# Performance work log

Hardware: AMD Instinct MI355X
Metric: run time of the kernel (lower is better)

Reference implementation:

```python
import jax, jax.numpy as jnp
import numpy as np

N_NODES = 100000

def spmm(edge_row, edge_col, edge_val, dense):
    # sparse [N,N] @ dense [N,D] via gather + segment_sum
    msgs = edge_val[:, None] * dense[edge_col]          # [E, D]
    return jax.ops.segment_sum(msgs, edge_row, num_segments=N_NODES)

def setup_inputs() -> dict:
    key = jax.random.key(0)
    ks = jax.random.split(key, 6)
    N, F, H, C, E = N_NODES, 512, 256, 40, 3200000
    x = jax.random.normal(ks[0], (N, F), dtype=jnp.float32)
    edge_row = jax.random.randint(ks[1], (E,), 0, N, dtype=jnp.int32)
    edge_col = jax.random.randint(ks[2], (E,), 0, N, dtype=jnp.int32)
    edge_val = jax.random.uniform(ks[3], (E,), dtype=jnp.float32)
    # xavier_uniform init for conv weights, zeros for biases
    lim1 = float(np.sqrt(6.0 / (F + H)))
    lim2 = float(np.sqrt(6.0 / (H + C)))
    W1 = jax.random.uniform(ks[4], (F, H), minval=-lim1, maxval=lim1, dtype=jnp.float32)
    b1 = jnp.zeros((H,), dtype=jnp.float32)
    W2 = jax.random.uniform(ks[5], (H, C), minval=-lim2, maxval=lim2, dtype=jnp.float32)
    b2 = jnp.zeros((C,), dtype=jnp.float32)
    return {"x": x, "edge_row": edge_row, "edge_col": edge_col, "edge_val": edge_val,
            "W1": W1, "b1": b1, "W2": W2, "b2": b2}

def reference(x, edge_row, edge_col, edge_val, W1, b1, W2, b2):
    # layer 1: dense transform, sparse aggregation, bias, relu (dropout = identity in eval)
    h = spmm(edge_row, edge_col, edge_val, x @ W1) + b1   # [N, H]
    h = jax.nn.relu(h)
    mid = h
    # layer 2
    out = spmm(edge_row, edge_col, edge_val, h @ W2) + b2  # [N, C]
    return (mid, out)  # out.squeeze(1) is a no-op for C>1
```

## Files before the change

### kernel.cpp

```cpp
#include <hip/hip_runtime.h>


typedef __bf16 bf16;
typedef __bf16 bf16x8 __attribute__((ext_vector_type(8)));
typedef float floatx4 __attribute__((ext_vector_type(4)));
typedef float floatx2 __attribute__((ext_vector_type(2)));

#define NBMAX 400

__device__ __forceinline__ float bflo(unsigned int u) { return __uint_as_float(u << 16); }
__device__ __forceinline__ float bfhi(unsigned int u) { return __uint_as_float(u & 0xffff0000u); }

__global__ __launch_bounds__(256) void conv_w(const float* __restrict__ W1,
                                              const float* __restrict__ W2,
                                              bf16* __restrict__ W1T,
                                              bf16* __restrict__ W2T) {
  int i = blockIdx.x * 256 + threadIdx.x;
  if (i < 512 * 256) {
    int k = i >> 8, n = i & 255;
    W1T[n * 512 + k] = (bf16)W1[i];
  }
  int j = i - 512 * 256;
  if (j >= 0 && j < 48 * 256) {
    int n = j >> 8, k = j & 255;
    W2T[j] = (n < 40) ? (bf16)W2[k * 40 + n] : (bf16)0.0f;
  }
}

__global__ __launch_bounds__(256) void cvt_fp8_kernel(const unsigned int* __restrict__ in,
                                                      unsigned int* __restrict__ out,
                                                      int n8) {
  int i = blockIdx.x * 256 + threadIdx.x;
  if (i >= n8) return;
  uint4 u = ((const uint4*)in)[i];
  int p0 = 0, p1 = 0;
  p0 = __builtin_amdgcn_cvt_pk_fp8_f32(bflo(u.x), bfhi(u.x), p0, false);
  p0 = __builtin_amdgcn_cvt_pk_fp8_f32(bflo(u.y), bfhi(u.y), p0, true);
  p1 = __builtin_amdgcn_cvt_pk_fp8_f32(bflo(u.z), bfhi(u.z), p1, false);
  p1 = __builtin_amdgcn_cvt_pk_fp8_f32(bflo(u.w), bfhi(u.w), p1, true);
  ((uint2*)out)[i] = make_uint2((unsigned int)p0, (unsigned int)p1);
}

__global__ __launch_bounds__(256) void bhist_kernel(const int* __restrict__ er,
                                                    int* __restrict__ gbcount,
                                                    int E, int NB) {
  __shared__ int cnt[NBMAX];
  const int t = threadIdx.x;
  for (int b = t; b < NB; b += 256) cnt[b] = 0;
  __syncthreads();
  const int base = blockIdx.x * 8192;
#pragma unroll
  for (int k = 0; k < 8; k++) {
    int i = base + k * 1024 + t * 4;
    if (i < E) {
      int4 r = *(const int4*)(er + i);
      atomicAdd(&cnt[r.x >> 8], 1);
      atomicAdd(&cnt[r.y >> 8], 1);
      atomicAdd(&cnt[r.z >> 8], 1);
      atomicAdd(&cnt[r.w >> 8], 1);
    }
  }
  __syncthreads();
  for (int b = t; b < NB; b += 256)
    if (cnt[b]) atomicAdd(&gbcount[b], cnt[b]);
}

__global__ __launch_bounds__(512) void bscan_kernel(const int* __restrict__ gbcount,
                                                    int* __restrict__ bstart,
                                                    int* __restrict__ bcur, int NB) {
  __shared__ int wsum[8];
  const int t = threadIdx.x;
  const int lane = t & 63, wave = t >> 6;
  int v = (t < NB) ? gbcount[t] : 0;
  int incl = v;
#pragma unroll
  for (int d = 1; d < 64; d <<= 1) {
    int o = __shfl_up(incl, d, 64);
    if (lane >= d) incl += o;
  }
  if (lane == 63) wsum[wave] = incl;
  __syncthreads();
  int off = 0;
#pragma unroll
  for (int w = 0; w < 8; w++)
    if (w < wave) off += wsum[w];
  int excl = off + incl - v;
  if (t <= NB) bstart[t] = excl;
  if (t < NB) bcur[t] = excl;
}

__global__ __launch_bounds__(256) void partA_kernel(
    const int* __restrict__ er, const int* __restrict__ ec, const float* __restrict__ ev,
    int* __restrict__ bcur, int2* __restrict__ epack_b, int E, int NB) {
  __shared__ int cnt[NBMAX];
  __shared__ int cur[NBMAX];
  const int t = threadIdx.x;
  for (int b = t; b < NB; b += 256) cnt[b] = 0;
  __syncthreads();
  const int base = blockIdx.x * 8192;
#pragma unroll
  for (int k = 0; k < 8; k++) {
    int i = base + k * 1024 + t * 4;
    if (i < E) {
      int4 r = *(const int4*)(er + i);
      atomicAdd(&cnt[r.x >> 8], 1);
      atomicAdd(&cnt[r.y >> 8], 1);
      atomicAdd(&cnt[r.z >> 8], 1);
      atomicAdd(&cnt[r.w >> 8], 1);
    }
  }
  __syncthreads();
  for (int b = t; b < NB; b += 256)
    cur[b] = cnt[b] ? atomicAdd(&bcur[b], cnt[b]) : 0;
  __syncthreads();
#pragma unroll
  for (int k = 0; k < 8; k++) {
    int i = base + k * 1024 + t * 4;
    if (i < E) {
      int4 r = *(const int4*)(er + i);
      int4 c = *(const int4*)(ec + i);
      float4 v = *(const float4*)(ev + i);
      int s0 = atomicAdd(&cur[r.x >> 8], 1);
      epack_b[s0] = make_int2(((r.x & 255) << 17) | c.x, __float_as_int(v.x));
      int s1 = atomicAdd(&cur[r.y >> 8], 1);
      epack_b[s1] = make_int2(((r.y & 255) << 17) | c.y, __float_as_int(v.y));
      int s2 = atomicAdd(&cur[r.z >> 8], 1);
      epack_b[s2] = make_int2(((r.z & 255) << 17) | c.z, __float_as_int(v.z));
      int s3 = atomicAdd(&cur[r.w >> 8], 1);
      epack_b[s3] = make_int2(((r.w & 255) << 17) | c.w, __float_as_int(v.w));
    }
  }
}

__global__ __launch_bounds__(256) void partB_kernel(
    const int2* __restrict__ epack_b, const int* __restrict__ bstart,
    int2* __restrict__ epack_f, int* __restrict__ rp, int M) {
  __shared__ int rcnt[256];
  __shared__ int rcur[256];
  __shared__ int wsum[4];
  const int b = blockIdx.x, t = threadIdx.x;
  const int s = bstart[b];
  const int e_ = bstart[b + 1];
  rcnt[t] = 0;
  __syncthreads();
  for (int i = s + t; i < e_; i += 256) {
    unsigned int ro = ((unsigned int)epack_b[i].x) >> 17;
    atomicAdd(&rcnt[ro], 1);
  }
  __syncthreads();
  const int lane = t & 63, wave = t >> 6;
  int v = rcnt[t];
  int incl = v;
#pragma unroll
  for (int d = 1; d < 64; d <<= 1) {
    int o = __shfl_up(incl, d, 64);
    if (lane >= d) incl += o;
  }
  if (lane == 63) wsum[wave] = incl;
  __syncthreads();
  int off = 0;
#pragma unroll
  for (int w = 0; w < 4; w++)
    if (w < wave) off += wsum[w];
  rcur[t] = s + off + incl - v;
  __syncthreads();
  for (int i = s + t; i < e_; i += 256) {
    int2 m = epack_b[i];
    unsigned int ro = ((unsigned int)m.x) >> 17;
    int slot = atomicAdd(&rcur[ro], 1);
    epack_f[slot] = make_int2(m.x & 0x1FFFF, m.y);
  }
  __syncthreads();
  int r = (b << 8) + t;
  if (r < M) rp[r] = rcur[t];
}

__global__ __launch_bounds__(256) void gemm1_kernel(const float* __restrict__ x,
                                                    const bf16* __restrict__ W1T,
                                                    bf16* __restrict__ T1, int M) {
  __shared__ __align__(16) bf16 As[64][40];
  __shared__ __align__(16) bf16 Bs[256][40];
  const int t = threadIdx.x;
  const int wave = t >> 6, lane = t & 63;
  const int quad = lane >> 4, l16 = lane & 15;
  const int m0 = blockIdx.x * 64;
  floatx4 acc[16] = {};

  const int ar = t >> 2, aq = t & 3;
  const int a_gr = m0 + ar;
  const float* a_src = x + (size_t)a_gr * 512 + aq * 8;
  const bf16* b_src = W1T + (size_t)t * 512;

  for (int k0 = 0; k0 < 512; k0 += 32) {
    __syncthreads();
    {
      float4 f0 = {0,0,0,0}, f1 = {0,0,0,0};
      if (a_gr < M) {
        const float4* p = (const float4*)(a_src + k0);
        f0 = p[0]; f1 = p[1];
      }
      bf16x8 av;
      av[0] = (bf16)f0.x; av[1] = (bf16)f0.y; av[2] = (bf16)f0.z; av[3] = (bf16)f0.w;
      av[4] = (bf16)f1.x; av[5] = (bf16)f1.y; av[6] = (bf16)f1.z; av[7] = (bf16)f1.w;
      *(bf16x8*)&As[ar][aq * 8] = av;
    }
    {
      const bf16* p = b_src + k0;
      bf16x8 q0 = *(const bf16x8*)(p);
      bf16x8 q1 = *(const bf16x8*)(p + 8);
      bf16x8 q2 = *(const bf16x8*)(p + 16);
      bf16x8 q3 = *(const bf16x8*)(p + 24);
      *(bf16x8*)&Bs[t][0]  = q0;
      *(bf16x8*)&Bs[t][8]  = q1;
      *(bf16x8*)&Bs[t][16] = q2;
      *(bf16x8*)&Bs[t][24] = q3;
    }
    __syncthreads();
    bf16x8 a = *(const bf16x8*)&As[wave * 16 + l16][quad * 8];
#pragma unroll
    for (int nt = 0; nt < 16; nt++) {
      bf16x8 b = *(const bf16x8*)&Bs[nt * 16 + l16][quad * 8];
      acc[nt] = __builtin_amdgcn_mfma_f32_16x16x32_bf16(a, b, acc[nt], 0, 0, 0);
    }
  }
  const int row_base = m0 + wave * 16 + quad * 4;
#pragma unroll
  for (int nt = 0; nt < 16; nt++) {
#pragma unroll
    for (int j = 0; j < 4; j++) {
      int gr = row_base + j;
      if (gr < M) T1[(size_t)gr * 256 + nt * 16 + l16] = (bf16)acc[nt][j];
    }
  }
}

__global__ __launch_bounds__(256) void spmm1_kernel(
    const int* __restrict__ rp, const int2* __restrict__ epack,
    const unsigned int* __restrict__ T1f8, const float* __restrict__ b1,
    float* __restrict__ mid, int M) {
  const int lane = threadIdx.x & 63;
  const int r = blockIdx.x * 4 + (threadIdx.x >> 6);
  if (r >= M) return;
  const int eend = rp[r];
  int e = (r == 0) ? 0 : rp[r - 1];
  float a0 = 0.f, a1 = 0.f, a2 = 0.f, a3 = 0.f;
  const unsigned int* base = T1f8 + lane;
  if (e < eend && (e & 1)) {
    int2 m = epack[e];
    float v = __int_as_float(m.y);
    unsigned int u = base[(size_t)m.x * 64];
    floatx2 lo = __builtin_amdgcn_cvt_pk_f32_fp8(u, false);
    floatx2 hi = __builtin_amdgcn_cvt_pk_f32_fp8(u, true);
    a0 += v * lo[0]; a1 += v * lo[1]; a2 += v * hi[0]; a3 += v * hi[1];
    e++;
  }
  for (; e + 3 < eend; e += 4) {
    int4 p01 = *(const int4*)(epack + e);
    int4 p23 = *(const int4*)(epack + e + 2);
    unsigned int u0 = base[(size_t)p01.x * 64];
    unsigned int u1 = base[(size_t)p01.z * 64];
    unsigned int u2 = base[(size_t)p23.x * 64];
    unsigned int u3 = base[(size_t)p23.z * 64];
    float v0 = __int_as_float(p01.y), v1 = __int_as_float(p01.w);
    float v2 = __int_as_float(p23.y), v3 = __int_as_float(p23.w);
    floatx2 l0 = __builtin_amdgcn_cvt_pk_f32_fp8(u0, false);
    floatx2 h0 = __builtin_amdgcn_cvt_pk_f32_fp8(u0, true);
    floatx2 l1 = __builtin_amdgcn_cvt_pk_f32_fp8(u1, false);
    floatx2 h1 = __builtin_amdgcn_cvt_pk_f32_fp8(u1, true);
    floatx2 l2 = __builtin_amdgcn_cvt_pk_f32_fp8(u2, false);
    floatx2 h2 = __builtin_amdgcn_cvt_pk_f32_fp8(u2, true);
    floatx2 l3 = __builtin_amdgcn_cvt_pk_f32_fp8(u3, false);
    floatx2 h3 = __builtin_amdgcn_cvt_pk_f32_fp8(u3, true);
    a0 += v0 * l0[0]; a1 += v0 * l0[1]; a2 += v0 * h0[0]; a3 += v0 * h0[1];
    a0 += v1 * l1[0]; a1 += v1 * l1[1]; a2 += v1 * h1[0]; a3 += v1 * h1[1];
    a0 += v2 * l2[0]; a1 += v2 * l2[1]; a2 += v2 * h2[0]; a3 += v2 * h2[1];
    a0 += v3 * l3[0]; a1 += v3 * l3[1]; a2 += v3 * h3[0]; a3 += v3 * h3[1];
  }
  for (; e < eend; e++) {
    int2 m = epack[e];
    float v = __int_as_float(m.y);
    unsigned int u = base[(size_t)m.x * 64];
    floatx2 lo = __builtin_amdgcn_cvt_pk_f32_fp8(u, false);
    floatx2 hi = __builtin_amdgcn_cvt_pk_f32_fp8(u, true);
    a0 += v * lo[0]; a1 += v * lo[1]; a2 += v * hi[0]; a3 += v * hi[1];
  }
  int c = lane * 4;
  float4 bb = *(const float4*)(b1 + c);
  float4 o;
  o.x = fmaxf(a0 + bb.x, 0.f);
  o.y = fmaxf(a1 + bb.y, 0.f);
  o.z = fmaxf(a2 + bb.z, 0.f);
  o.w = fmaxf(a3 + bb.w, 0.f);
  *(float4*)(mid + (size_t)r * 256 + c) = o;
}

__global__ __launch_bounds__(256) void gemm2_kernel(const float* __restrict__ mid,
                                                    const bf16* __restrict__ W2T,
                                                    bf16* __restrict__ T2p, int M) {
  __shared__ __align__(16) bf16 As[64][40];
  __shared__ __align__(16) bf16 Bs[48][40];
  const int t = threadIdx.x;
  const int wave = t >> 6, lane = t & 63;
  const int quad = lane >> 4, l16 = lane & 15;
  const int m0 = blockIdx.x * 64;
  floatx4 acc[3] = {};
  const int ar = t >> 2, aq = t & 3;
  const int a_gr = m0 + ar;
  const float* a_src = mid + (size_t)a_gr * 256 + aq * 8;

  for (int k0 = 0; k0 < 256; k0 += 32) {
    __syncthreads();
    {
      float4 f0 = {0,0,0,0}, f1 = {0,0,0,0};
      if (a_gr < M) {
        const float4* p = (const float4*)(a_src + k0);
        f0 = p[0]; f1 = p[1];
      }
      bf16x8 av;
      av[0] = (bf16)f0.x; av[1] = (bf16)f0.y; av[2] = (bf16)f0.z; av[3] = (bf16)f0.w;
      av[4] = (bf16)f1.x; av[5] = (bf16)f1.y; av[6] = (bf16)f1.z; av[7] = (bf16)f1.w;
      *(bf16x8*)&As[ar][aq * 8] = av;
    }
    if (t < 192) {
      int n = t >> 2, q = t & 3;
      bf16x8 b = *(const bf16x8*)(W2T + n * 256 + k0 + q * 8);
      *(bf16x8*)&Bs[n][q * 8] = b;
    }
    __syncthreads();
    bf16x8 a = *(const bf16x8*)&As[wave * 16 + l16][quad * 8];
#pragma unroll
    for (int nt = 0; nt < 3; nt++) {
      bf16x8 b = *(const bf16x8*)&Bs[nt * 16 + l16][quad * 8];
      acc[nt] = __builtin_amdgcn_mfma_f32_16x16x32_bf16(a, b, acc[nt], 0, 0, 0);
    }
  }
  const int row_base = m0 + wave * 16 + quad * 4;
#pragma unroll
  for (int nt = 0; nt < 3; nt++) {
#pragma unroll
    for (int j = 0; j < 4; j++) {
      int gr = row_base + j;
      int col = nt * 16 + l16;
      if (gr < M && col < 40) T2p[(size_t)gr * 64 + col] = (bf16)acc[nt][j];
    }
  }
}

__global__ __launch_bounds__(256) void spmm2_kernel(
    const int* __restrict__ rp, const int2* __restrict__ epack,
    const unsigned int* __restrict__ T2f8, const float* __restrict__ b2,
    float* __restrict__ out2, int M) {
  const int lane = threadIdx.x & 63;
  const int r = blockIdx.x * 4 + (threadIdx.x >> 6);
  if (r >= M) return;
  const int q = lane & 15;
  const int g = lane >> 4;
  const int eend = rp[r];
  int e = (r == 0) ? 0 : rp[r - 1];
  float a0 = 0.f, a1 = 0.f, a2 = 0.f, a3 = 0.f;
  const unsigned int* base = T2f8 + q;
  for (; e + 3 < eend; e += 4) {
    int2 m = epack[e + g];
    float v = __int_as_float(m.y);
    unsigned int u = base[(size_t)m.x * 16];
    floatx2 lo = __builtin_amdgcn_cvt_pk_f32_fp8(u, false);
    floatx2 hi = __builtin_amdgcn_cvt_pk_f32_fp8(u, true);
    a0 += v * lo[0]; a1 += v * lo[1]; a2 += v * hi[0]; a3 += v * hi[1];
  }
  if (e + g < eend) {
    int2 m = epack[e + g];
    float v = __int_as_float(m.y);
    unsigned int u = base[(size_t)m.x * 16];
    floatx2 lo = __builtin_amdgcn_cvt_pk_f32_fp8(u, false);
    floatx2 hi = __builtin_amdgcn_cvt_pk_f32_fp8(u, true);
    a0 += v * lo[0]; a1 += v * lo[1]; a2 += v * hi[0]; a3 += v * hi[1];
  }
  a0 += __shfl_down(a0, 32, 64); a0 += __shfl_down(a0, 16, 64);
  a1 += __shfl_down(a1, 32, 64); a1 += __shfl_down(a1, 16, 64);
  a2 += __shfl_down(a2, 32, 64); a2 += __shfl_down(a2, 16, 64);
  a3 += __shfl_down(a3, 32, 64); a3 += __shfl_down(a3, 16, 64);
  if (lane < 10) {
    int c = lane * 4;
    float4 o;
    o.x = a0 + b2[c];
    o.y = a1 + b2[c + 1];
    o.z = a2 + b2[c + 2];
    o.w = a3 + b2[c + 3];
    *(float4*)(out2 + (size_t)r * 40 + c) = o;
  }
}

extern "C" void kernel_launch(void* const* d_in, const int* in_sizes, int n_in,
                              void* d_out, int out_size, void* d_ws, size_t ws_size,
                              hipStream_t stream) {
  const float* x        = (const float*)d_in[0];
  const int*   edge_row = (const int*)d_in[1];
  const int*   edge_col = (const int*)d_in[2];
  const float* edge_val = (const float*)d_in[3];
  const float* W1       = (const float*)d_in[4];
  const float* b1       = (const float*)d_in[5];
  const float* W2       = (const float*)d_in[6];
  const float* b2       = (const float*)d_in[7];
  const int M = in_sizes[0] / 512;
  const int E = in_sizes[1];
  const int NB = (M + 255) >> 8;

  char* ws = (char*)d_ws;
  size_t off = 0;
  bf16* T1      = (bf16*)(ws + off);  off += (size_t)M * 256 * 2;
  bf16* W1T     = (bf16*)(ws + off);  off += 512 * 256 * 2;
  bf16* W2T     = (bf16*)(ws + off);  off += 48 * 256 * 2;
  bf16* T2p     = (bf16*)(ws + off);  off += (size_t)M * 64 * 2;
  unsigned int* T1f8 = (unsigned int*)(ws + off); off += (size_t)M * 256;
  unsigned int* T2f8 = (unsigned int*)(ws + off); off += (size_t)M * 64;
  int* rp       = (int*)(ws + off);   off += (size_t)M * 4;
  int* gbcount  = (int*)(ws + off);   off += NBMAX * 4;
  int* bstart   = (int*)(ws + off);   off += (NBMAX + 1) * 4;
  int* bcur     = (int*)(ws + off);   off += NBMAX * 4;
  off = (off + 15) & ~(size_t)15;
  int2* epack_f = (int2*)(ws + off);  off += (size_t)E * 8;
  int2* epack_b = (int2*)T1;

  float* mid  = (float*)d_out;
  float* out2 = mid + (size_t)M * 256;

  const int EBLK = (E + 8191) / 8192;

  hipMemsetAsync(gbcount, 0, NBMAX * 4, stream);
  conv_w<<<(512 * 256 + 48 * 256 + 255) / 256, 256, 0, stream>>>(W1, W2, W1T, W2T);
  bhist_kernel<<<EBLK, 256, 0, stream>>>(edge_row, gbcount, E, NB);
  bscan_kernel<<<1, 512, 0, stream>>>(gbcount, bstart, bcur, NB);
  partA_kernel<<<EBLK, 256, 0, stream>>>(edge_row, edge_col, edge_val,
                                         bcur, epack_b, E, NB);
  partB_kernel<<<NB, 256, 0, stream>>>(epack_b, bstart, epack_f, rp, M);
  gemm1_kernel<<<(M + 63) / 64, 256, 0, stream>>>(x, W1T, T1, M);
  {
    int n8 = M * 256 / 8;
    cvt_fp8_kernel<<<(n8 + 255) / 256, 256, 0, stream>>>((const unsigned int*)T1,
                                                         T1f8, n8);
  }
  spmm1_kernel<<<(M + 3) / 4, 256, 0, stream>>>(rp, epack_f, T1f8, b1, mid, M);
  gemm2_kernel<<<(M + 63) / 64, 256, 0, stream>>>(mid, W2T, T2p, M);
  {
    int n8 = M * 64 / 8;
    cvt_fp8_kernel<<<(n8 + 255) / 256, 256, 0, stream>>>((const unsigned int*)T2p,
                                                         T2f8, n8);
  }
  spmm2_kernel<<<(M + 3) / 4, 256, 0, stream>>>(rp, epack_f, T2f8, b2, out2, M);
}
```

Measured before the change: 737.6 us.

## Precompute per-block bucket offsets and unroll SpMM gather loops further

New measurement: 691.4 us. 6.3% less time.

```diff
diff --git a/kernel.cpp b/kernel.cpp
--- a/kernel.cpp
+++ b/kernel.cpp
@@ -43,7 +43,8 @@
 
 __global__ __launch_bounds__(256) void bhist_kernel(const int* __restrict__ er,
                                                     int* __restrict__ gbcount,
-                                                    int E, int NB) {
+                                                    int* __restrict__ blkcnt,
+                                                    int E, int NB, int EBLK) {
   __shared__ int cnt[NBMAX];
   const int t = threadIdx.x;
   for (int b = t; b < NB; b += 256) cnt[b] = 0;
@@ -61,13 +62,15 @@
     }
   }
   __syncthreads();
-  for (int b = t; b < NB; b += 256)
-    if (cnt[b]) atomicAdd(&gbcount[b], cnt[b]);
+  for (int b = t; b < NB; b += 256) {
+    int c = cnt[b];
+    blkcnt[b * EBLK + blockIdx.x] = c;
+    if (c) atomicAdd(&gbcount[b], c);
+  }
 }
 
 __global__ __launch_bounds__(512) void bscan_kernel(const int* __restrict__ gbcount,
-                                                    int* __restrict__ bstart,
-                                                    int* __restrict__ bcur, int NB) {
+                                                    int* __restrict__ bstart, int NB) {
   __shared__ int wsum[8];
   const int t = threadIdx.x;
   const int lane = t & 63, wave = t >> 6;
@@ -86,33 +89,38 @@
     if (w < wave) off += wsum[w];
   int excl = off + incl - v;
   if (t <= NB) bstart[t] = excl;
-  if (t < NB) bcur[t] = excl;
+}
+
+__global__ __launch_bounds__(512) void bscan2_kernel(const int* __restrict__ blkcnt,
+                                                     const int* __restrict__ bstart,
+                                                     int* __restrict__ blkoff, int EBLK) {
+  __shared__ int wsum[8];
+  const int b = blockIdx.x, t = threadIdx.x;
+  const int lane = t & 63, wave = t >> 6;
+  int v = (t < EBLK) ? blkcnt[b * EBLK + t] : 0;
+  int incl = v;
+#pragma unroll
+  for (int d = 1; d < 64; d <<= 1) {
+    int o = __shfl_up(incl, d, 64);
+    if (lane >= d) incl += o;
+  }
+  if (lane == 63) wsum[wave] = incl;
+  __syncthreads();
+  int off = 0;
+#pragma unroll
+  for (int w = 0; w < 8; w++)
+    if (w < wave) off += wsum[w];
+  if (t < EBLK) blkoff[b * EBLK + t] = bstart[b] + off + incl - v;
 }
 
 __global__ __launch_bounds__(256) void partA_kernel(
     const int* __restrict__ er, const int* __restrict__ ec, const float* __restrict__ ev,
-    int* __restrict__ bcur, int2* __restrict__ epack_b, int E, int NB) {
-  __shared__ int cnt[NBMAX];
+    const int* __restrict__ blkoff, int2* __restrict__ epack_b, int E, int NB, int EBLK) {
   __shared__ int cur[NBMAX];
   const int t = threadIdx.x;
-  for (int b = t; b < NB; b += 256) cnt[b] = 0;
+  for (int b = t; b < NB; b += 256) cur[b] = blkoff[b * EBLK + blockIdx.x];
   __syncthreads();
   const int base = blockIdx.x * 8192;
-#pragma unroll
-  for (int k = 0; k < 8; k++) {
-    int i = base + k * 1024 + t * 4;
-    if (i < E) {
-      int4 r = *(const int4*)(er + i);
-      atomicAdd(&cnt[r.x >> 8], 1);
-      atomicAdd(&cnt[r.y >> 8], 1);
-      atomicAdd(&cnt[r.z >> 8], 1);
-      atomicAdd(&cnt[r.w >> 8], 1);
-    }
-  }
-  __syncthreads();
-  for (int b = t; b < NB; b += 256)
-    cur[b] = cnt[b] ? atomicAdd(&bcur[b], cnt[b]) : 0;
-  __syncthreads();
 #pragma unroll
   for (int k = 0; k < 8; k++) {
     int i = base + k * 1024 + t * 4;
@@ -253,6 +261,48 @@
     floatx2 hi = __builtin_amdgcn_cvt_pk_f32_fp8(u, true);
     a0 += v * lo[0]; a1 += v * lo[1]; a2 += v * hi[0]; a3 += v * hi[1];
     e++;
+  }
+  for (; e + 7 < eend; e += 8) {
+    int4 p01 = *(const int4*)(epack + e);
+    int4 p23 = *(const int4*)(epack + e + 2);
+    int4 p45 = *(const int4*)(epack + e + 4);
+    int4 p67 = *(const int4*)(epack + e + 6);
+    unsigned int u0 = base[(size_t)p01.x * 64];
+    unsigned int u1 = base[(size_t)p01.z * 64];
+    unsigned int u2 = base[(size_t)p23.x * 64];
+    unsigned int u3 = base[(size_t)p23.z * 64];
+    unsigned int u4 = base[(size_t)p45.x * 64];
+    unsigned int u5 = base[(size_t)p45.z * 64];
+    unsigned int u6 = base[(size_t)p67.x * 64];
+    unsigned int u7 = base[(size_t)p67.z * 64];
+    float v0 = __int_as_float(p01.y), v1 = __int_as_float(p01.w);
+    float v2 = __int_as_float(p23.y), v3 = __int_as_float(p23.w);
+    float v4 = __int_as_float(p45.y), v5 = __int_as_float(p45.w);
+    float v6 = __int_as_float(p67.y), v7 = __int_as_float(p67.w);
+    floatx2 l0 = __builtin_amdgcn_cvt_pk_f32_fp8(u0, false);
+    floatx2 h0 = __builtin_amdgcn_cvt_pk_f32_fp8(u0, true);
+    floatx2 l1 = __builtin_amdgcn_cvt_pk_f32_fp8(u1, false);
+    floatx2 h1 = __builtin_amdgcn_cvt_pk_f32_fp8(u1, true);
+    floatx2 l2 = __builtin_amdgcn_cvt_pk_f32_fp8(u2, false);
+    floatx2 h2 = __builtin_amdgcn_cvt_pk_f32_fp8(u2, true);
+    floatx2 l3 = __builtin_amdgcn_cvt_pk_f32_fp8(u3, false);
+    floatx2 h3 = __builtin_amdgcn_cvt_pk_f32_fp8(u3, true);
+    floatx2 l4 = __builtin_amdgcn_cvt_pk_f32_fp8(u4, false);
+    floatx2 h4 = __builtin_amdgcn_cvt_pk_f32_fp8(u4, true);
+    floatx2 l5 = __builtin_amdgcn_cvt_pk_f32_fp8(u5, false);
+    floatx2 h5 = __builtin_amdgcn_cvt_pk_f32_fp8(u5, true);
+    floatx2 l6 = __builtin_amdgcn_cvt_pk_f32_fp8(u6, false);
+    floatx2 h6 = __builtin_amdgcn_cvt_pk_f32_fp8(u6, true);
+    floatx2 l7 = __builtin_amdgcn_cvt_pk_f32_fp8(u7, false);
+    floatx2 h7 = __builtin_amdgcn_cvt_pk_f32_fp8(u7, true);
+    a0 += v0 * l0[0]; a1 += v0 * l0[1]; a2 += v0 * h0[0]; a3 += v0 * h0[1];
+    a0 += v1 * l1[0]; a1 += v1 * l1[1]; a2 += v1 * h1[0]; a3 += v1 * h1[1];
+    a0 += v2 * l2[0]; a1 += v2 * l2[1]; a2 += v2 * h2[0]; a3 += v2 * h2[1];
+    a0 += v3 * l3[0]; a1 += v3 * l3[1]; a2 += v3 * h3[0]; a3 += v3 * h3[1];
+    a0 += v4 * l4[0]; a1 += v4 * l4[1]; a2 += v4 * h4[0]; a3 += v4 * h4[1];
+    a0 += v5 * l5[0]; a1 += v5 * l5[1]; a2 += v5 * h5[0]; a3 += v5 * h5[1];
+    a0 += v6 * l6[0]; a1 += v6 * l6[1]; a2 += v6 * h6[0]; a3 += v6 * h6[1];
+    a0 += v7 * l7[0]; a1 += v7 * l7[1]; a2 += v7 * h7[0]; a3 += v7 * h7[1];
   }
   for (; e + 3 < eend; e += 4) {
     int4 p01 = *(const int4*)(epack + e);
@@ -359,6 +409,29 @@
   int e = (r == 0) ? 0 : rp[r - 1];
   float a0 = 0.f, a1 = 0.f, a2 = 0.f, a3 = 0.f;
   const unsigned int* base = T2f8 + q;
+  if (e < eend && (e & 1)) {
+    if (g == 0) {
+      int2 m = epack[e];
+      float v = __int_as_float(m.y);
+      unsigned int u = base[(size_t)m.x * 16];
+      floatx2 lo = __builtin_amdgcn_cvt_pk_f32_fp8(u, false);
+      floatx2 hi = __builtin_amdgcn_cvt_pk_f32_fp8(u, true);
+      a0 += v * lo[0]; a1 += v * lo[1]; a2 += v * hi[0]; a3 += v * hi[1];
+    }
+    e++;
+  }
+  for (; e + 7 < eend; e += 8) {
+    int4 m = *(const int4*)(epack + e + 2 * g);
+    float v0 = __int_as_float(m.y), v1 = __int_as_float(m.w);
+    unsigned int u0 = base[(size_t)m.x * 16];
+    unsigned int u1 = base[(size_t)m.z * 16];
+    floatx2 l0 = __builtin_amdgcn_cvt_pk_f32_fp8(u0, false);
+    floatx2 h0 = __builtin_amdgcn_cvt_pk_f32_fp8(u0, true);
+    floatx2 l1 = __builtin_amdgcn_cvt_pk_f32_fp8(u1, false);
+    floatx2 h1 = __builtin_amdgcn_cvt_pk_f32_fp8(u1, true);
+    a0 += v0 * l0[0]; a1 += v0 * l0[1]; a2 += v0 * h0[0]; a3 += v0 * h0[1];
+    a0 += v1 * l1[0]; a1 += v1 * l1[1]; a2 += v1 * h1[0]; a3 += v1 * h1[1];
+  }
   for (; e + 3 < eend; e += 4) {
     int2 m = epack[e + g];
     float v = __int_as_float(m.y);
@@ -404,6 +477,7 @@
   const int M = in_sizes[0] / 512;
   const int E = in_sizes[1];
   const int NB = (M + 255) >> 8;
+  const int EBLK = (E + 8191) / 8192;
 
   char* ws = (char*)d_ws;
   size_t off = 0;
@@ -416,7 +490,8 @@
   int* rp       = (int*)(ws + off);   off += (size_t)M * 4;
   int* gbcount  = (int*)(ws + off);   off += NBMAX * 4;
   int* bstart   = (int*)(ws + off);   off += (NBMAX + 1) * 4;
-  int* bcur     = (int*)(ws + off);   off += NBMAX * 4;
+  int* blkcnt   = (int*)(ws + off);   off += (size_t)NB * EBLK * 4;
+  int* blkoff   = (int*)(ws + off);   off += (size_t)NB * EBLK * 4;
   off = (off + 15) & ~(size_t)15;
   int2* epack_f = (int2*)(ws + off);  off += (size_t)E * 8;
   int2* epack_b = (int2*)T1;
@@ -424,14 +499,13 @@
   float* mid  = (float*)d_out;
   float* out2 = mid + (size_t)M * 256;
 
-  const int EBLK = (E + 8191) / 8192;
-
   hipMemsetAsync(gbcount, 0, NBMAX * 4, stream);
   conv_w<<<(512 * 256 + 48 * 256 + 255) / 256, 256, 0, stream>>>(W1, W2, W1T, W2T);
-  bhist_kernel<<<EBLK, 256, 0, stream>>>(edge_row, gbcount, E, NB);
-  bscan_kernel<<<1, 512, 0, stream>>>(gbcount, bstart, bcur, NB);
+  bhist_kernel<<<EBLK, 256, 0, stream>>>(edge_row, gbcount, blkcnt, E, NB, EBLK);
+  bscan_kernel<<<1, 512, 0, stream>>>(gbcount, bstart, NB);
+  bscan2_kernel<<<NB, 512, 0, stream>>>(blkcnt, bstart, blkoff, EBLK);
   partA_kernel<<<EBLK, 256, 0, stream>>>(edge_row, edge_col, edge_val,
-                                         bcur, epack_b, E, NB);
+                                         blkoff, epack_b, E, NB, EBLK);
   partB_kernel<<<NB, 256, 0, stream>>>(epack_b, bstart, epack_f, rp, M);
   gemm1_kernel<<<(M + 63) / 64, 256, 0, stream>>>(x, W1T, T1, M);
   {
```
